# Kernel optimization log

Measured on AMD Instinct MI355X. Metric: run time of the kernel, lower is better.

## Reference

```python
import jax, jax.numpy as jnp
import numpy as np

TOP_K = 2
NUM_EXPERTS = 64
AUX_LOSS_COEF = 0.01
Z_LOSS_COEF = 0.001


def setup_inputs() -> dict:
    key = jax.random.key(0)
    k1, k2 = jax.random.split(key)
    x = jax.random.normal(k1, (4, 8192, 4096), dtype=jnp.float32)
    gate_w = jax.random.normal(k2, (64, 4096), dtype=jnp.float32) * (1.0 / np.sqrt(4096))
    return {"x": x, "gate_w": gate_w}


def reference(x, gate_w):
    # gate linear (no bias): (B,S,D) @ (D,E) -> (B,S,E)
    router_logits = jnp.einsum("bsd,ed->bse", x, gate_w)
    B, S, E = router_logits.shape
    num_tokens = B * S

    # top-k selection + softmax over selected logits
    top_k_logits, top_k_indices = jax.lax.top_k(router_logits, TOP_K)
    top_k_weights = jax.nn.softmax(top_k_logits, axis=-1)

    # aux losses
    router_probs = jax.nn.softmax(router_logits, axis=-1)
    # tokens_per_expert: scatter-add of ones instead of materializing one-hot mask
    tokens_per_expert = (
        jnp.zeros((E,), dtype=jnp.float32)
        .at[top_k_indices.reshape(-1)]
        .add(1.0)
        / num_tokens
    )
    router_prob_per_expert = router_probs.mean(axis=(0, 1))
    balance_loss = (tokens_per_expert * router_prob_per_expert).sum() * E * AUX_LOSS_COEF
    z_loss = (jax.nn.logsumexp(router_logits, axis=-1).mean() ** 2) * Z_LOSS_COEF

    return (top_k_indices, top_k_weights, balance_loss, z_loss, tokens_per_expert)
```

## Files before the change

### kernel.cpp

```cpp
#include <hip/hip_runtime.h>
#include <math.h>

#define D 4096
#define E_EXPERTS 64
#define NTOK 32768
#define BM 64
#define NTHREADS 256
#define NKT 128
#define L_LD 65
#define SMEM_FLOATS 6144
#define TAU 2.5e-4f
#define WP_OFF 4096
#define WPLANE 524288


typedef float f32x4 __attribute__((ext_vector_type(4)));
typedef short short8v __attribute__((ext_vector_type(8)));

__device__ __forceinline__ unsigned short f2bf_rne(float f) {
  unsigned u = __builtin_bit_cast(unsigned, f);
  unsigned r = (u + 0x7fffu + ((u >> 16) & 1u)) >> 16;
  return (unsigned short)r;
}
__device__ __forceinline__ float bf2f(unsigned short h) {
  unsigned u = ((unsigned)h) << 16;
  return __builtin_bit_cast(float, u);
}

__device__ __forceinline__ void split8(float4 a, float4 b, short8v* h,
                                       short8v* l) {
  float f[8] = {a.x, a.y, a.z, a.w, b.x, b.y, b.z, b.w};
  short8v hv, lv;
#pragma unroll
  for (int i = 0; i < 8; ++i) {
    unsigned short hs = f2bf_rne(f[i]);
    float rem = f[i] - bf2f(hs);
    hv[i] = (short)hs;
    lv[i] = (short)f2bf_rne(rem);
  }
  *h = hv;
  *l = lv;
}

__global__ __launch_bounds__(256)
void prep_w(const float* __restrict__ gw, unsigned short* __restrict__ wph) {
  unsigned short* wpl = wph + (WPLANE / 2);
  int i = blockIdx.x * 256 + threadIdx.x;
  int e = i >> 10;
  int k = (i & 1023) << 2;
  float4 v = *(const float4*)(gw + (size_t)e * D + k);
  float f[4] = {v.x, v.y, v.z, v.w};
  int kt = k >> 5, oct = (k >> 3) & 3, k8 = k & 7;
  size_t base = (size_t)kt * 2048 + (size_t)(oct * 64 + e) * 8 + k8;
  unsigned long long ph = 0ull, pl = 0ull;
#pragma unroll
  for (int j = 0; j < 4; ++j) {
    unsigned short hs = f2bf_rne(f[j]);
    unsigned short ls = f2bf_rne(f[j] - bf2f(hs));
    ph |= (unsigned long long)hs << (16 * j);
    pl |= (unsigned long long)ls << (16 * j);
  }
  *(unsigned long long*)(wph + base) = ph;
  *(unsigned long long*)(wpl + base) = pl;
}

__global__ __launch_bounds__(NTHREADS)
void moe_router_main(const float* __restrict__ x,
                     const float* __restrict__ gw,
                     const char* __restrict__ wp,
                     float* __restrict__ out, float* __restrict__ ws) {
  __shared__ __align__(16) float smem[SMEM_FLOATS];
  char* sb = (char*)smem;

  const int tid = threadIdx.x;
  const int bid = blockIdx.x;
  const int t0 = bid * BM;
  const int w = tid >> 6;
  const int l = tid & 63;
  const int c4 = l >> 4, rb = l & 15;

  const size_t aOff = ((size_t)(t0 + w * 16 + rb)) * D + c4 * 8;
  int boff[4];
#pragma unroll
  for (int n = 0; n < 4; ++n) boff[n] = c4 * 1024 + (n * 16 + rb) * 16;

  const char* wpl = wp + WPLANE;

  f32x4 acc[4];
#pragma unroll
  for (int n = 0; n < 4; ++n) acc[n] = (f32x4){0.f, 0.f, 0.f, 0.f};

#define LOAD_A(PA, kt)                                   \
  {                                                      \
    PA[0] = *(const float4*)(x + aOff + (kt)*32);        \
    PA[1] = *(const float4*)(x + aOff + (kt)*32 + 4);    \
  }
#define LOAD_B(kt)                                                 \
  {                                                                \
    bvh = *(const float4*)(wp + (size_t)(kt)*4096 + tid * 16);     \
    bvl = *(const float4*)(wpl + (size_t)(kt)*4096 + tid * 16);    \
  }
#define WRITE_B(bufb)                                    \
  {                                                      \
    *(float4*)(sb + (bufb) + tid * 16) = bvh;            \
    *(float4*)(sb + (bufb) + 4096 + tid * 16) = bvl;     \
  }
#define COMPUTE(bufb, ah, al)                                                  \
  {                                                                            \
    _Pragma("unroll") for (int n = 0; n < 4; ++n) {                            \
      short8v bh = *(const short8v*)(sb + (bufb) + boff[n]);                   \
      short8v bl = *(const short8v*)(sb + (bufb) + 4096 + boff[n]);            \
      acc[n] = __builtin_amdgcn_mfma_f32_16x16x32_bf16(ah, bh, acc[n], 0, 0, 0); \
      acc[n] = __builtin_amdgcn_mfma_f32_16x16x32_bf16(ah, bl, acc[n], 0, 0, 0); \
      acc[n] = __builtin_amdgcn_mfma_f32_16x16x32_bf16(al, bh, acc[n], 0, 0, 0); \
    }                                                                          \
  }
#define ITER(PA, kt)                          \
  {                                           \
    short8v ah, al;                           \
    split8(PA[0], PA[1], &ah, &al);           \
    if ((kt) + 2 < NKT) {                     \
      LOAD_A(PA, (kt) + 2);                   \
      LOAD_B((kt) + 2);                       \
    }                                         \
    COMPUTE(bc * 8192, ah, al);               \
    if ((kt) + 2 < NKT) WRITE_B(bt * 8192);   \
    __syncthreads();                          \
    bc = bc == 2 ? 0 : bc + 1;                \
    bt = bt == 2 ? 0 : bt + 1;                \
  }

  float4 paA[2], paB[2], bvh, bvl;
  LOAD_A(paA, 0);
  LOAD_A(paB, 1);
  LOAD_B(0);
  WRITE_B(0);
  LOAD_B(1);
  WRITE_B(8192);
  __syncthreads();

  int bc = 0, bt = 2;
  for (int kt = 0; kt < NKT; kt += 2) {
    ITER(paA, kt);
    ITER(paB, kt + 1);
  }

#pragma unroll
  for (int n = 0; n < 4; ++n)
#pragma unroll
    for (int r = 0; r < 4; ++r) {
      int row = w * 16 + c4 * 4 + r;
      int col = n * 16 + rb;
      smem[row * L_LD + col] = acc[n][r];
    }

  float* L = smem;
  float* mArr = smem + BM * L_LD;
  float* zArr = mArr + BM;
  float* cntL = zArr + BM;
  float* probA = cntL + E_EXPERTS;
  if (tid < E_EXPERTS) {
    cntL[tid] = 0.0f;
    probA[tid] = 0.0f;
  }
  __syncthreads();

  if (tid < BM) {
    const int lane = tid;
    const float* row = L + tid * L_LD;
    float m1 = -3.4e38f, m2 = -3.4e38f, m3 = -3.4e38f;
    int i1 = 0, i2 = 0, i3 = 0;
    for (int e = 0; e < E_EXPERTS; ++e) {
      float v = row[e];
      if (v > m1) {
        m3 = m2; i3 = i2;
        m2 = m1; i2 = i1;
        m1 = v;  i1 = e;
      } else if (v > m2) {
        m3 = m2; i3 = i2;
        m2 = v;  i2 = e;
      } else if (v > m3) {
        m3 = v; i3 = e;
      }
    }
    float z = 0.0f;
    for (int e = 0; e < E_EXPERTS; ++e) z += __expf(row[e] - m1);
    mArr[tid] = m1;
    zArr[tid] = 1.0f / z;
    float lseVal = m1 + logf(z);

    bool risky = (m1 - m2 < TAU) || (m2 - m3 < TAU);
    double r1 = 0.0, r2 = 0.0, r3 = 0.0;
    unsigned long long mask = __ballot(risky);
    while (mask) {
      int src = __ffsll((long long)mask) - 1;
      mask &= (mask - 1);
      int tok = t0 + src;
      int j1 = __shfl(i1, src, 64);
      int j2 = __shfl(i2, src, 64);
      int j3 = __shfl(i3, src, 64);
      const float* xr = x + (size_t)tok * D;
      const float* g1 = gw + (size_t)j1 * D;
      const float* g2 = gw + (size_t)j2 * D;
      const float* g3 = gw + (size_t)j3 * D;
      double a1 = 0.0, a2 = 0.0, a3 = 0.0;
      for (int k = lane * 4; k < D; k += 256) {
        float4 xv = *(const float4*)(xr + k);
        float4 w1 = *(const float4*)(g1 + k);
        float4 w2 = *(const float4*)(g2 + k);
        float4 w3 = *(const float4*)(g3 + k);
        a1 += (double)xv.x * w1.x + (double)xv.y * w1.y +
              (double)xv.z * w1.z + (double)xv.w * w1.w;
        a2 += (double)xv.x * w2.x + (double)xv.y * w2.y +
              (double)xv.z * w2.z + (double)xv.w * w2.w;
        a3 += (double)xv.x * w3.x + (double)xv.y * w3.y +
              (double)xv.z * w3.z + (double)xv.w * w3.w;
      }
#pragma unroll
      for (int off = 32; off > 0; off >>= 1) {
        a1 += __shfl_down(a1, off, 64);
        a2 += __shfl_down(a2, off, 64);
        a3 += __shfl_down(a3, off, 64);
      }
      a1 = __shfl(a1, 0, 64);
      a2 = __shfl(a2, 0, 64);
      a3 = __shfl(a3, 0, 64);
      if (lane == src) { r1 = a1; r2 = a2; r3 = a3; }
    }

    float wOut1, wOut2;
    if (risky) {
      double v[3] = {r1, r2, r3};
      int ix[3] = {i1, i2, i3};
#define SORT_SWAP(a, b)                                            \
      if (v[b] > v[a] || (v[b] == v[a] && ix[b] < ix[a])) {        \
        double tv = v[a]; v[a] = v[b]; v[b] = tv;                  \
        int ti = ix[a]; ix[a] = ix[b]; ix[b] = ti;                 \
      }
      SORT_SWAP(0, 1);
      SORT_SWAP(1, 2);
      SORT_SWAP(0, 1);
#undef SORT_SWAP
      i1 = ix[0]; i2 = ix[1];
      double d = exp(v[1] - v[0]);
      wOut1 = (float)(1.0 / (1.0 + d));
      wOut2 = (float)(d / (1.0 + d));
    } else {
      float e2 = __expf(m2 - m1);
      wOut1 = 1.0f / (1.0f + e2);
      wOut2 = e2 * wOut1;
    }

    size_t ot = ((size_t)t0 + tid) * 2;
    out[ot] = (float)i1;
    out[ot + 1] = (float)i2;
    out[(size_t)NTOK * 2 + ot] = wOut1;
    out[(size_t)NTOK * 2 + ot + 1] = wOut2;

    atomicAdd(&cntL[i1], 1.0f);
    atomicAdd(&cntL[i2], 1.0f);

    float v = lseVal;
#pragma unroll
    for (int off = 32; off > 0; off >>= 1) v += __shfl_down(v, off, 64);
    if (tid == 0) atomicAdd(&ws[128], v);
  }
  __syncthreads();
  if (tid < E_EXPERTS) atomicAdd(&ws[tid], cntL[tid]);

  {
    const int e = tid & 63;
    const int q = tid >> 6;
    float s = 0.0f;
    for (int t = q * 16; t < q * 16 + 16; ++t)
      s += __expf(L[t * L_LD + e] - mArr[t]) * zArr[t];
    atomicAdd(&probA[e], s);
  }
  __syncthreads();
  if (tid < E_EXPERTS) atomicAdd(&ws[64 + tid], probA[tid]);
}

__global__ void moe_finalize(const float* __restrict__ ws,
                             float* __restrict__ out) {
  const int e = threadIdx.x;
  const float inv_n = 1.0f / (float)NTOK;
  float tpe = ws[e] * inv_n;
  out[131074 + e] = tpe;
  float rppe = ws[64 + e] * inv_n;
  float part = tpe * rppe;
#pragma unroll
  for (int off = 32; off > 0; off >>= 1) part += __shfl_down(part, off, 64);
  if (e == 0) {
    out[131072] = part * 64.0f * 0.01f;
    float meanLse = ws[128] * inv_n;
    out[131073] = meanLse * meanLse * 0.001f;
  }
}

extern "C" void kernel_launch(void* const* d_in, const int* in_sizes, int n_in,
                              void* d_out, int out_size, void* d_ws, size_t ws_size,
                              hipStream_t stream) {
  const float* x = (const float*)d_in[0];
  const float* gw = (const float*)d_in[1];
  float* out = (float*)d_out;
  float* ws = (float*)d_ws;
  unsigned short* wph = (unsigned short*)((char*)d_ws + WP_OFF);

  hipMemsetAsync(d_ws, 0, 129 * sizeof(float), stream);
  hipLaunchKernelGGL(prep_w, dim3(256), dim3(256), 0, stream, gw, wph);
  hipLaunchKernelGGL(moe_router_main, dim3(NTOK / BM), dim3(NTHREADS), 0, stream,
                     x, gw, (const char*)wph, out, ws);
  hipLaunchKernelGGL(moe_finalize, dim3(1), dim3(E_EXPERTS), 0, stream, ws, out);
}
```

Before: 187.5 us.

## Load gate weight fragments directly from global into registers, drop LDS staging

```diff
diff --git a/kernel.cpp b/kernel.cpp
--- a/kernel.cpp
+++ b/kernel.cpp
@@ -8,7 +8,7 @@
 #define NTHREADS 256
 #define NKT 128
 #define L_LD 65
-#define SMEM_FLOATS 6144
+#define SMEM_FLOATS 4608
 #define TAU 2.5e-4f
 #define WP_OFF 4096
 #define WPLANE 524288
@@ -70,7 +70,6 @@
                      const char* __restrict__ wp,
                      float* __restrict__ out, float* __restrict__ ws) {
   __shared__ __align__(16) float smem[SMEM_FLOATS];
-  char* sb = (char*)smem;
 
   const int tid = threadIdx.x;
   const int bid = blockIdx.x;
@@ -90,59 +89,52 @@
 #pragma unroll
   for (int n = 0; n < 4; ++n) acc[n] = (f32x4){0.f, 0.f, 0.f, 0.f};
 
-#define LOAD_A(PA, kt)                                   \
-  {                                                      \
-    PA[0] = *(const float4*)(x + aOff + (kt)*32);        \
-    PA[1] = *(const float4*)(x + aOff + (kt)*32 + 4);    \
-  }
-#define LOAD_B(kt)                                                 \
-  {                                                                \
-    bvh = *(const float4*)(wp + (size_t)(kt)*4096 + tid * 16);     \
-    bvl = *(const float4*)(wpl + (size_t)(kt)*4096 + tid * 16);    \
-  }
-#define WRITE_B(bufb)                                    \
-  {                                                      \
-    *(float4*)(sb + (bufb) + tid * 16) = bvh;            \
-    *(float4*)(sb + (bufb) + 4096 + tid * 16) = bvl;     \
-  }
-#define COMPUTE(bufb, ah, al)                                                  \
+#define LOAD_A(PA, kt)                                 \
+  {                                                    \
+    PA[0] = *(const float4*)(x + aOff + (kt)*32);      \
+    PA[1] = *(const float4*)(x + aOff + (kt)*32 + 4);  \
+  }
+#define LOAD_B(BH, BL, kt)                                                    \
+  {                                                                           \
+    const char* tb_ = wp + (size_t)(kt)*4096;                                 \
+    const char* tl_ = wpl + (size_t)(kt)*4096;                                \
+    _Pragma("unroll") for (int n = 0; n < 4; ++n) {                           \
+      BH[n] = *(const short8v*)(tb_ + boff[n]);                               \
+      BL[n] = *(const short8v*)(tl_ + boff[n]);                               \
+    }                                                                         \
+  }
+#define COMPUTE_SET(PA, BH, BL)                                                \
   {                                                                            \
+    short8v ah, al;                                                            \
+    split8(PA[0], PA[1], &ah, &al);                                            \
     _Pragma("unroll") for (int n = 0; n < 4; ++n) {                            \
-      short8v bh = *(const short8v*)(sb + (bufb) + boff[n]);                   \
-      short8v bl = *(const short8v*)(sb + (bufb) + 4096 + boff[n]);            \
-      acc[n] = __builtin_amdgcn_mfma_f32_16x16x32_bf16(ah, bh, acc[n], 0, 0, 0); \
-      acc[n] = __builtin_amdgcn_mfma_f32_16x16x32_bf16(ah, bl, acc[n], 0, 0, 0); \
-      acc[n] = __builtin_amdgcn_mfma_f32_16x16x32_bf16(al, bh, acc[n], 0, 0, 0); \
+      acc[n] =                                                                 \
+          __builtin_amdgcn_mfma_f32_16x16x32_bf16(ah, BH[n], acc[n], 0, 0, 0); \
+      acc[n] =                                                                 \
+          __builtin_amdgcn_mfma_f32_16x16x32_bf16(ah, BL[n], acc[n], 0, 0, 0); \
+      acc[n] =                                                                 \
+          __builtin_amdgcn_mfma_f32_16x16x32_bf16(al, BH[n], acc[n], 0, 0, 0); \
     }                                                                          \
   }
-#define ITER(PA, kt)                          \
-  {                                           \
-    short8v ah, al;                           \
-    split8(PA[0], PA[1], &ah, &al);           \
-    if ((kt) + 2 < NKT) {                     \
-      LOAD_A(PA, (kt) + 2);                   \
-      LOAD_B((kt) + 2);                       \
-    }                                         \
-    COMPUTE(bc * 8192, ah, al);               \
-    if ((kt) + 2 < NKT) WRITE_B(bt * 8192);   \
-    __syncthreads();                          \
-    bc = bc == 2 ? 0 : bc + 1;                \
-    bt = bt == 2 ? 0 : bt + 1;                \
-  }
-
-  float4 paA[2], paB[2], bvh, bvl;
-  LOAD_A(paA, 0);
-  LOAD_A(paB, 1);
-  LOAD_B(0);
-  WRITE_B(0);
-  LOAD_B(1);
-  WRITE_B(8192);
-  __syncthreads();
-
-  int bc = 0, bt = 2;
+
+  float4 pa0[2], pa1[2];
+  short8v bh0[4], bl0[4], bh1[4], bl1[4];
+  LOAD_A(pa0, 0);
+  LOAD_B(bh0, bl0, 0);
+  LOAD_A(pa1, 1);
+  LOAD_B(bh1, bl1, 1);
+
   for (int kt = 0; kt < NKT; kt += 2) {
-    ITER(paA, kt);
-    ITER(paB, kt + 1);
+    COMPUTE_SET(pa0, bh0, bl0);
+    if (kt + 2 < NKT) {
+      LOAD_A(pa0, kt + 2);
+      LOAD_B(bh0, bl0, kt + 2);
+    }
+    COMPUTE_SET(pa1, bh1, bl1);
+    if (kt + 3 < NKT) {
+      LOAD_A(pa1, kt + 3);
+      LOAD_B(bh1, bl1, kt + 3);
+    }
   }
 
 #pragma unroll
```

New measurement: 220.3 us. 1.18x slower.
